# Optimization experiments

Hardware: AMD Instinct MI355X
Metric: run time of the kernel (lower is better)

Reference implementation:

```python
import jax, jax.numpy as jnp
import numpy as np

NUM_HEADS = 8
EPS = 1e-12  # torch F.normalize eps


def _l2norm(t):
    n = jnp.linalg.norm(t, axis=-1, keepdims=True)
    return t / jnp.maximum(n, EPS)


def setup_inputs() -> dict:
    key = jax.random.key(0)
    ks = jax.random.split(key, 8)
    b, hw, c = 1, 4096, 64
    scale = 1.0 / np.sqrt(c)
    return {
        "x": jax.random.normal(ks[0], (b, hw, c), jnp.float32),
        "y": jax.random.normal(ks[1], (b, hw, c), jnp.float32),
        "Wq": jax.random.normal(ks[2], (c, c), jnp.float32) * scale,
        "bq": jax.random.normal(ks[3], (c,), jnp.float32) * 0.02,
        "Wkv": jax.random.normal(ks[4], (c, 2 * c), jnp.float32) * scale,
        "bkv": jax.random.normal(ks[5], (2 * c,), jnp.float32) * 0.02,
        "We": jax.random.normal(ks[6], (c, c), jnp.float32) * scale,
        "be": jax.random.normal(ks[7], (c,), jnp.float32) * 0.02,
    }


def reference(x, y, Wq, bq, Wkv, bkv, We, be):
    b, hw, c = x.shape
    H = NUM_HEADS
    d = c // H

    # q projection -> [b, H, hw, d]
    q = (x @ Wq + bq).reshape(b, hw, H, d).transpose(0, 2, 1, 3)
    # kv projection -> k, v each [b, H, hw, d]
    kv = (y @ Wkv + bkv).reshape(b, hw, 2, H, d)
    k = kv[:, :, 0].transpose(0, 2, 1, 3)
    v = kv[:, :, 1].transpose(0, 2, 1, 3)

    # cosine-normalized attention (no 1/sqrt(d) scale in original)
    q = _l2norm(q)
    k = _l2norm(k)
    attn = jnp.einsum("bhqd,bhkd->bhqk", q, k)  # [b, H, hw, hw]
    attn = jax.nn.softmax(attn, axis=-1)
    out = jnp.einsum("bhqk,bhkd->bhqd", attn, v)  # [b, H, hw, d]

    # merge heads -> [b, hw, c], then output projection
    out = out.transpose(0, 2, 1, 3).reshape(b, hw, c)
    return out @ We + be
```

## Files before the change

### kernel.cpp

```cpp
#include <hip/hip_runtime.h>

#define HW 4096
#define C 64
#define H 8
#define D 8
#define L2E 1.44269504088896340736f

typedef _Float16 h2 __attribute__((ext_vector_type(2)));
typedef _Float16 half4 __attribute__((ext_vector_type(4)));
typedef float f32x4 __attribute__((ext_vector_type(4)));

static __device__ __forceinline__ float fdot2(h2 a, h2 b, float c) {
    return __builtin_amdgcn_fdot2(a, b, c, false);
}

static __device__ __forceinline__ float fast_exp2(float x) {
#if __has_builtin(__builtin_amdgcn_exp2f)
    return __builtin_amdgcn_exp2f(x);
#else
    return __exp2f(x);
#endif
}

static __device__ __forceinline__ h2 pack_h2(float a, float b) {
    return __builtin_bit_cast(h2, __builtin_amdgcn_cvt_pkrtz(a, b));
}

static __device__ __forceinline__ half4 cat_h2(h2 lo, h2 hi) {
    uint2 u;
    u.x = __builtin_bit_cast(unsigned, lo);
    u.y = __builtin_bit_cast(unsigned, hi);
    return __builtin_bit_cast(half4, u);
}

static __device__ __forceinline__ f32x4 mfma16(half4 a, half4 b, f32x4 c) {
    return __builtin_amdgcn_mfma_f32_16x16x16f16(a, b, c, 0, 0, 0);
}

static __device__ __forceinline__ float gnorm8(float a) {
    float ss = a * a;
    ss += __shfl_xor(ss, 1, 64);
    ss += __shfl_xor(ss, 2, 64);
    ss += __shfl_xor(ss, 4, 64);
    return 1.0f / fmaxf(sqrtf(ss), 1e-12f);
}

__global__ __launch_bounds__(192) void proj_kernel(
    const float* __restrict__ x, const float* __restrict__ y,
    const float* __restrict__ Wq, const float* __restrict__ bq,
    const float* __restrict__ Wkv, const float* __restrict__ bkv,
    _Float16* __restrict__ qh, _Float16* __restrict__ kh, _Float16* __restrict__ vt)
{
    const int r0 = blockIdx.x * 4;
    const int wave = __builtin_amdgcn_readfirstlane((int)(threadIdx.x >> 6));
    const int j = threadIdx.x & 63;

    const float* __restrict__ W;
    const float* __restrict__ rows;
    int wstride;
    float bias;
    if (wave == 0)      { W = Wq + j;        wstride = C;     bias = bq[j];      rows = x + (size_t)r0 * C; }
    else if (wave == 1) { W = Wkv + j;       wstride = 2 * C; bias = bkv[j];     rows = y + (size_t)r0 * C; }
    else                { W = Wkv + C + j;   wstride = 2 * C; bias = bkv[C + j]; rows = y + (size_t)r0 * C; }

    float a0 = bias, a1 = bias, a2 = bias, a3 = bias;
    #pragma unroll
    for (int i = 0; i < C; ++i) {
        const float w = W[(size_t)i * wstride];
        a0 = fmaf(rows[i],         w, a0);
        a1 = fmaf(rows[C + i],     w, a1);
        a2 = fmaf(rows[2 * C + i], w, a2);
        a3 = fmaf(rows[3 * C + i], w, a3);
    }

    const int head = j >> 3;
    const int d = j & 7;
    if (wave == 0) {
        const float s0 = gnorm8(a0) * L2E, s1 = gnorm8(a1) * L2E;
        const float s2 = gnorm8(a2) * L2E, s3 = gnorm8(a3) * L2E;
        _Float16* p = qh + ((size_t)head * HW + r0) * D + d;
        p[0 * D] = (_Float16)(a0 * s0);
        p[1 * D] = (_Float16)(a1 * s1);
        p[2 * D] = (_Float16)(a2 * s2);
        p[3 * D] = (_Float16)(a3 * s3);
    } else if (wave == 1) {
        const float s0 = gnorm8(a0), s1 = gnorm8(a1);
        const float s2 = gnorm8(a2), s3 = gnorm8(a3);
        _Float16* p = kh + ((size_t)head * HW + r0) * D + d;
        p[0 * D] = (_Float16)(a0 * s0);
        p[1 * D] = (_Float16)(a1 * s1);
        p[2 * D] = (_Float16)(a2 * s2);
        p[3 * D] = (_Float16)(a3 * s3);
    } else {
        const h2 lo = pack_h2(a0, a1);
        const h2 hi = pack_h2(a2, a3);
        *(half4*)(vt + (size_t)j * HW + r0) = cat_h2(lo, hi);
    }
}

__global__ __launch_bounds__(512, 8) void attn_kernel(
    const _Float16* __restrict__ qh, const _Float16* __restrict__ kh,
    const _Float16* __restrict__ vt, float* __restrict__ Ofin)
{
    const int split = __builtin_amdgcn_readfirstlane((int)(threadIdx.x >> 6));
    const int lane = threadIdx.x & 63;
    const int n = lane & 15;
    const int quad = lane >> 4;
    const int h = blockIdx.x & 7;
    const int qp = blockIdx.x >> 3;
    const int q0 = qp * 32;

    const _Float16* __restrict__ qhh = qh + (size_t)h * HW * D;
    const _Float16* __restrict__ khh = kh + (size_t)h * HW * D;
    const _Float16* __restrict__ vth = vt + (size_t)h * D * HW;

    const half4 z4 = {};
    half4 qf0 = z4, qf1 = z4;
    if (quad < 2) {
        qf0 = *(const half4*)(qhh + (size_t)(q0 + n) * D + quad * 4);
        qf1 = *(const half4*)(qhh + (size_t)(q0 + 16 + n) * D + quad * 4);
    }

    f32x4 o0 = {}, o1 = {};
    float l0 = 0.f, l1 = 0.f;
    const h2 one2 = { (_Float16)1.0f, (_Float16)1.0f };

    const int kt0 = split * 32;
    #pragma unroll 4
    for (int t = 0; t < 32; ++t) {
        const int kbase = (kt0 + t) * 16;
        half4 kf = *(const half4*)(khh + (size_t)(kbase + n) * D + (quad & 1) * 4);
        kf = (quad < 2) ? kf : z4;
        half4 vf = *(const half4*)(vth + (size_t)(n & 7) * HW + kbase + quad * 4);
        vf = (n < 8) ? vf : z4;

        const f32x4 zc = {};
        f32x4 c0 = mfma16(kf, qf0, zc);
        f32x4 c1 = mfma16(kf, qf1, zc);

        const float pa0 = fast_exp2(c0[0]), pa1 = fast_exp2(c0[1]);
        const float pa2 = fast_exp2(c0[2]), pa3 = fast_exp2(c0[3]);
        const h2 lo0 = pack_h2(pa0, pa1), hi0 = pack_h2(pa2, pa3);
        l0 = fdot2(lo0, one2, l0);
        l0 = fdot2(hi0, one2, l0);
        const half4 pb0 = cat_h2(lo0, hi0);

        const float pb0e = fast_exp2(c1[0]), pb1e = fast_exp2(c1[1]);
        const float pb2e = fast_exp2(c1[2]), pb3e = fast_exp2(c1[3]);
        const h2 lo1 = pack_h2(pb0e, pb1e), hi1 = pack_h2(pb2e, pb3e);
        l1 = fdot2(lo1, one2, l1);
        l1 = fdot2(hi1, one2, l1);
        const half4 pb1 = cat_h2(lo1, hi1);

        o0 = mfma16(vf, pb0, o0);
        o1 = mfma16(vf, pb1, o1);
    }

    l0 += __shfl_xor(l0, 16, 64); l0 += __shfl_xor(l0, 32, 64);
    l1 += __shfl_xor(l1, 16, 64); l1 += __shfl_xor(l1, 32, 64);

    __shared__ float sO[8][2][16][8];
    __shared__ float sL[8][2][16];
    if (quad < 2) {
        *(float4*)&sO[split][0][n][quad * 4] = make_float4(o0[0], o0[1], o0[2], o0[3]);
        *(float4*)&sO[split][1][n][quad * 4] = make_float4(o1[0], o1[1], o1[2], o1[3]);
    }
    if (lane < 16)      sL[split][0][lane]      = l0;
    else if (lane < 32) sL[split][1][lane - 16] = l1;
    __syncthreads();

    const int t = threadIdx.x;
    if (t < 256) {
        const int tile = t >> 7;
        const int n2 = (t >> 3) & 15;
        const int d2 = t & 7;
        float os = 0.f, ls = 0.f;
        #pragma unroll
        for (int s2 = 0; s2 < 8; ++s2) {
            os += sO[s2][tile][n2][d2];
            ls += sL[s2][tile][n2];
        }
        Ofin[((size_t)h * HW + q0 + tile * 16 + n2) * D + d2] = os / ls;
    }
}

__global__ __launch_bounds__(256) void outproj_kernel(
    const float* __restrict__ Ofin, const float* __restrict__ We,
    const float* __restrict__ be, float* __restrict__ out)
{
    const int t = threadIdx.x;
    const int wave = __builtin_amdgcn_readfirstlane((int)(t >> 6));
    const int lane = t & 63;
    const int rbase = blockIdx.x * 16 + wave * 4;
    const int head = lane >> 3;
    const int d = lane & 7;

    __shared__ float sO[16][64];

    #pragma unroll
    for (int rr = 0; rr < 4; ++rr) {
        const int r = rbase + rr;
        sO[wave * 4 + rr][lane] = Ofin[((size_t)head * HW + r) * D + d];
    }
    __syncthreads();

    const float bias = be[lane];
    float a0 = bias, a1 = bias, a2 = bias, a3 = bias;
    #pragma unroll
    for (int i4 = 0; i4 < 16; ++i4) {
        const int i = i4 * 4;
        const float4 o0 = *(const float4*)&sO[wave * 4 + 0][i];
        const float4 o1 = *(const float4*)&sO[wave * 4 + 1][i];
        const float4 o2 = *(const float4*)&sO[wave * 4 + 2][i];
        const float4 o3 = *(const float4*)&sO[wave * 4 + 3][i];
        const float w0 = We[(size_t)(i + 0) * C + lane];
        const float w1 = We[(size_t)(i + 1) * C + lane];
        const float w2 = We[(size_t)(i + 2) * C + lane];
        const float w3 = We[(size_t)(i + 3) * C + lane];
        a0 = fmaf(o0.x, w0, a0); a0 = fmaf(o0.y, w1, a0); a0 = fmaf(o0.z, w2, a0); a0 = fmaf(o0.w, w3, a0);
        a1 = fmaf(o1.x, w0, a1); a1 = fmaf(o1.y, w1, a1); a1 = fmaf(o1.z, w2, a1); a1 = fmaf(o1.w, w3, a1);
        a2 = fmaf(o2.x, w0, a2); a2 = fmaf(o2.y, w1, a2); a2 = fmaf(o2.z, w2, a2); a2 = fmaf(o2.w, w3, a2);
        a3 = fmaf(o3.x, w0, a3); a3 = fmaf(o3.y, w1, a3); a3 = fmaf(o3.z, w2, a3); a3 = fmaf(o3.w, w3, a3);
    }
    out[(size_t)(rbase + 0) * C + lane] = a0;
    out[(size_t)(rbase + 1) * C + lane] = a1;
    out[(size_t)(rbase + 2) * C + lane] = a2;
    out[(size_t)(rbase + 3) * C + lane] = a3;
}

extern "C" void kernel_launch(void* const* d_in, const int* in_sizes, int n_in,
                              void* d_out, int out_size, void* d_ws, size_t ws_size,
                              hipStream_t stream) {
    const float* x   = (const float*)d_in[0];
    const float* y   = (const float*)d_in[1];
    const float* Wq  = (const float*)d_in[2];
    const float* bq  = (const float*)d_in[3];
    const float* Wkv = (const float*)d_in[4];
    const float* bkv = (const float*)d_in[5];
    const float* We  = (const float*)d_in[6];
    const float* be  = (const float*)d_in[7];
    float* out = (float*)d_out;

    char* ws = (char*)d_ws;
    _Float16* qh   = (_Float16*)(ws);
    _Float16* kh   = (_Float16*)(ws + (512u << 10));
    _Float16* vt   = (_Float16*)(ws + (1024u << 10));
    float*    Ofin = (float*)   (ws + (1536u << 10));

    hipLaunchKernelGGL(proj_kernel, dim3(HW / 4), dim3(192), 0, stream,
                       x, y, Wq, bq, Wkv, bkv, qh, kh, vt);
    hipLaunchKernelGGL(attn_kernel, dim3(H * (HW / 32)), dim3(512), 0, stream,
                       qh, kh, vt, Ofin);
    hipLaunchKernelGGL(outproj_kernel, dim3(HW / 16), dim3(256), 0, stream,
                       Ofin, We, be, out);
}
```

Baseline: 114.1 us.

## Stage K/V tiles in LDS, fold row-sum into MFMA, move split reduction to outproj

Each block now serves 8 waves covering 256 queries against one 512-key split, and stages that split's K and V (plus a row of ones) in shared memory so all waves reuse it. The softmax denominator comes from the MFMA via the extra ones row instead of separate fdot2 accumulation. The cross-split reduction and normalization move out of the attention kernel into the output-projection kernel through partial-output workspace buffers. This removes redundant global K/V loads and the in-block reduction sync, in exchange for extra workspace traffic and more reads in outproj.

```diff
diff --git a/kernel.cpp b/kernel.cpp
--- a/kernel.cpp
+++ b/kernel.cpp
@@ -4,15 +4,15 @@
 #define C 64
 #define H 8
 #define D 8
+#define S 8
+#define KEYS_PER_SPLIT (HW / S)
+#define TILES (KEYS_PER_SPLIT / 16)
 #define L2E 1.44269504088896340736f
+#define VROW 1032
 
 typedef _Float16 h2 __attribute__((ext_vector_type(2)));
 typedef _Float16 half4 __attribute__((ext_vector_type(4)));
 typedef float f32x4 __attribute__((ext_vector_type(4)));
-
-static __device__ __forceinline__ float fdot2(h2 a, h2 b, float c) {
-    return __builtin_amdgcn_fdot2(a, b, c, false);
-}
 
 static __device__ __forceinline__ float fast_exp2(float x) {
 #if __has_builtin(__builtin_amdgcn_exp2f)
@@ -94,25 +94,48 @@
     } else {
         const h2 lo = pack_h2(a0, a1);
         const h2 hi = pack_h2(a2, a3);
-        *(half4*)(vt + (size_t)j * HW + r0) = cat_h2(lo, hi);
+        uint2 u;
+        u.x = __builtin_bit_cast(unsigned, lo);
+        u.y = __builtin_bit_cast(unsigned, hi);
+        *(half4*)(vt + (size_t)j * HW + r0) = __builtin_bit_cast(half4, u);
     }
 }
 
 __global__ __launch_bounds__(512, 8) void attn_kernel(
     const _Float16* __restrict__ qh, const _Float16* __restrict__ kh,
-    const _Float16* __restrict__ vt, float* __restrict__ Ofin)
+    const _Float16* __restrict__ vt, float* __restrict__ po, float* __restrict__ pl)
 {
-    const int split = __builtin_amdgcn_readfirstlane((int)(threadIdx.x >> 6));
-    const int lane = threadIdx.x & 63;
+    __shared__ __align__(16) char smem[512 * 16 + 16 * VROW];
+    char* sV = smem + 512 * 16;
+
+    const int tid = threadIdx.x;
+    const int wave = __builtin_amdgcn_readfirstlane(tid >> 6);
+    const int lane = tid & 63;
     const int n = lane & 15;
     const int quad = lane >> 4;
-    const int h = blockIdx.x & 7;
-    const int qp = blockIdx.x >> 3;
-    const int q0 = qp * 32;
+
+    const int b = blockIdx.x;
+    const int h = b & 7;
+    const int qg = (b >> 3) & 15;
+    const int split = b >> 7;
+    const int q0 = qg * 256 + wave * 32;
+    const int k0 = split * KEYS_PER_SPLIT;
 
     const _Float16* __restrict__ qhh = qh + (size_t)h * HW * D;
     const _Float16* __restrict__ khh = kh + (size_t)h * HW * D;
     const _Float16* __restrict__ vth = vt + (size_t)h * D * HW;
+
+    {
+        const uint4 kd = *(const uint4*)(khh + (size_t)(k0 + tid) * D);
+        *(uint4*)(smem + tid * 16) = kd;
+    }
+    {
+        const uint4 vd = *(const uint4*)(vth + (size_t)wave * HW + k0 + lane * 8);
+        char* dst = sV + wave * VROW + lane * 16;
+        *(uint2*)dst       = make_uint2(vd.x, vd.y);
+        *(uint2*)(dst + 8) = make_uint2(vd.z, vd.w);
+    }
+    if (tid < 256) *(unsigned*)(sV + 8 * VROW + tid * 4) = 0x3C003C00u;
 
     const half4 z4 = {};
     half4 qf0 = z4, qf1 = z4;
@@ -121,72 +144,41 @@
         qf1 = *(const half4*)(qhh + (size_t)(q0 + 16 + n) * D + quad * 4);
     }
 
+    __syncthreads();
+
     f32x4 o0 = {}, o1 = {};
-    float l0 = 0.f, l1 = 0.f;
-    const h2 one2 = { (_Float16)1.0f, (_Float16)1.0f };
-
-    const int kt0 = split * 32;
-    #pragma unroll 4
-    for (int t = 0; t < 32; ++t) {
-        const int kbase = (kt0 + t) * 16;
-        half4 kf = *(const half4*)(khh + (size_t)(kbase + n) * D + (quad & 1) * 4);
-        kf = (quad < 2) ? kf : z4;
-        half4 vf = *(const half4*)(vth + (size_t)(n & 7) * HW + kbase + quad * 4);
-        vf = (n < 8) ? vf : z4;
-
+    const int kOff = n * 16 + (quad & 1) * 8;
+    const int vOff = n * VROW + quad * 8;
+
+    #pragma unroll 8
+    for (int t = 0; t < TILES; ++t) {
+        const half4 kf = __builtin_bit_cast(half4, *(const uint2*)(smem + kOff + t * 256));
+        const half4 vf = __builtin_bit_cast(half4, *(const uint2*)(sV + vOff + t * 32));
         const f32x4 zc = {};
         f32x4 c0 = mfma16(kf, qf0, zc);
         f32x4 c1 = mfma16(kf, qf1, zc);
-
-        const float pa0 = fast_exp2(c0[0]), pa1 = fast_exp2(c0[1]);
-        const float pa2 = fast_exp2(c0[2]), pa3 = fast_exp2(c0[3]);
-        const h2 lo0 = pack_h2(pa0, pa1), hi0 = pack_h2(pa2, pa3);
-        l0 = fdot2(lo0, one2, l0);
-        l0 = fdot2(hi0, one2, l0);
-        const half4 pb0 = cat_h2(lo0, hi0);
-
-        const float pb0e = fast_exp2(c1[0]), pb1e = fast_exp2(c1[1]);
-        const float pb2e = fast_exp2(c1[2]), pb3e = fast_exp2(c1[3]);
-        const h2 lo1 = pack_h2(pb0e, pb1e), hi1 = pack_h2(pb2e, pb3e);
-        l1 = fdot2(lo1, one2, l1);
-        l1 = fdot2(hi1, one2, l1);
-        const half4 pb1 = cat_h2(lo1, hi1);
-
-        o0 = mfma16(vf, pb0, o0);
-        o1 = mfma16(vf, pb1, o1);
-    }
-
-    l0 += __shfl_xor(l0, 16, 64); l0 += __shfl_xor(l0, 32, 64);
-    l1 += __shfl_xor(l1, 16, 64); l1 += __shfl_xor(l1, 32, 64);
-
-    __shared__ float sO[8][2][16][8];
-    __shared__ float sL[8][2][16];
+        const h2 lo0 = pack_h2(fast_exp2(c0[0]), fast_exp2(c0[1]));
+        const h2 hi0 = pack_h2(fast_exp2(c0[2]), fast_exp2(c0[3]));
+        const h2 lo1 = pack_h2(fast_exp2(c1[0]), fast_exp2(c1[1]));
+        const h2 hi1 = pack_h2(fast_exp2(c1[2]), fast_exp2(c1[3]));
+        o0 = mfma16(vf, cat_h2(lo0, hi0), o0);
+        o1 = mfma16(vf, cat_h2(lo1, hi1), o1);
+    }
+
+    const size_t pbase = (size_t)(split * H + h) * HW;
     if (quad < 2) {
-        *(float4*)&sO[split][0][n][quad * 4] = make_float4(o0[0], o0[1], o0[2], o0[3]);
-        *(float4*)&sO[split][1][n][quad * 4] = make_float4(o1[0], o1[1], o1[2], o1[3]);
-    }
-    if (lane < 16)      sL[split][0][lane]      = l0;
-    else if (lane < 32) sL[split][1][lane - 16] = l1;
-    __syncthreads();
-
-    const int t = threadIdx.x;
-    if (t < 256) {
-        const int tile = t >> 7;
-        const int n2 = (t >> 3) & 15;
-        const int d2 = t & 7;
-        float os = 0.f, ls = 0.f;
-        #pragma unroll
-        for (int s2 = 0; s2 < 8; ++s2) {
-            os += sO[s2][tile][n2][d2];
-            ls += sL[s2][tile][n2];
-        }
-        Ofin[((size_t)h * HW + q0 + tile * 16 + n2) * D + d2] = os / ls;
+        *(float4*)(po + (pbase + q0 + n) * 8 + quad * 4)      = make_float4(o0[0], o0[1], o0[2], o0[3]);
+        *(float4*)(po + (pbase + q0 + 16 + n) * 8 + quad * 4) = make_float4(o1[0], o1[1], o1[2], o1[3]);
+    } else if (quad == 2) {
+        pl[pbase + q0 + n]      = o0[0];
+        pl[pbase + q0 + 16 + n] = o1[0];
     }
 }
 
 __global__ __launch_bounds__(256) void outproj_kernel(
-    const float* __restrict__ Ofin, const float* __restrict__ We,
-    const float* __restrict__ be, float* __restrict__ out)
+    const float* __restrict__ po, const float* __restrict__ pl,
+    const float* __restrict__ We, const float* __restrict__ be,
+    float* __restrict__ out)
 {
     const int t = threadIdx.x;
     const int wave = __builtin_amdgcn_readfirstlane((int)(t >> 6));
@@ -200,7 +192,13 @@
     #pragma unroll
     for (int rr = 0; rr < 4; ++rr) {
         const int r = rbase + rr;
-        sO[wave * 4 + rr][lane] = Ofin[((size_t)head * HW + r) * D + d];
+        float os = 0.f, ls = 0.f;
+        #pragma unroll
+        for (int s = 0; s < S; ++s) {
+            os += po[((size_t)(s * H + head) * HW + r) * 8 + d];
+            ls += pl[(size_t)(s * H + head) * HW + r];
+        }
+        sO[wave * 4 + rr][lane] = os / ls;
     }
     __syncthreads();
 
@@ -242,15 +240,16 @@
     float* out = (float*)d_out;
 
     char* ws = (char*)d_ws;
-    _Float16* qh   = (_Float16*)(ws);
-    _Float16* kh   = (_Float16*)(ws + (512u << 10));
-    _Float16* vt   = (_Float16*)(ws + (1024u << 10));
-    float*    Ofin = (float*)   (ws + (1536u << 10));
+    _Float16* qh = (_Float16*)(ws);
+    _Float16* kh = (_Float16*)(ws + (512u << 10));
+    _Float16* vt = (_Float16*)(ws + (1024u << 10));
+    float*    po = (float*)   (ws + (1536u << 10));
+    float*    pl = (float*)   (ws + (10240u << 10));
 
     hipLaunchKernelGGL(proj_kernel, dim3(HW / 4), dim3(192), 0, stream,
                        x, y, Wq, bq, Wkv, bkv, qh, kh, vt);
-    hipLaunchKernelGGL(attn_kernel, dim3(H * (HW / 32)), dim3(512), 0, stream,
-                       qh, kh, vt, Ofin);
+    hipLaunchKernelGGL(attn_kernel, dim3(H * (HW / 256) * S), dim3(512), 0, stream,
+                       qh, kh, vt, po, pl);
     hipLaunchKernelGGL(outproj_kernel, dim3(HW / 16), dim3(256), 0, stream,
-                       Ofin, We, be, out);
-}
+                       po, pl, We, be, out);
+}
```

Result: faster. 97.86 us (-14.2%).
